# Kernel optimization log

Hardware: AMD Instinct MI355X
Metric: run time of the kernel (lower is better)

## Reference

```python
import jax, jax.numpy as jnp
import numpy as np


def setup_inputs() -> dict:
    key = jax.random.key(0)
    kx, kq, kk, kv = jax.random.split(key, 4)
    B, S, D_IN, H, D_OUT = 2, 2048, 768, 12, 64
    scale = 0.02
    return {
        "x": jax.random.normal(kx, (B, S, D_IN), dtype=jnp.float32),
        "Wq": jax.random.normal(kq, (H, D_IN, D_OUT), dtype=jnp.float32) * scale,
        "Wk": jax.random.normal(kk, (H, D_IN, D_OUT), dtype=jnp.float32) * scale,
        "Wv": jax.random.normal(kv, (H, D_IN, D_OUT), dtype=jnp.float32) * scale,
    }


def reference(x, Wq, Wk, Wv):
    # x: [B, S, d_in]; Wq/Wk/Wv: [H, d_in, d_out] (stacked per-head Linear weights, no bias)
    B, S, _ = x.shape
    H, _, d_out = Wq.shape
    q = jnp.einsum("bsd,hde->bhse", x, Wq)  # [B, H, S, d_out]
    k = jnp.einsum("bsd,hde->bhse", x, Wk)
    v = jnp.einsum("bsd,hde->bhse", x, Wv)
    scores = jnp.einsum("bhse,bhte->bhst", q, k) / jnp.sqrt(jnp.float32(d_out))
    causal = jnp.tril(jnp.ones((S, S), dtype=bool))  # True = keep
    scores = jnp.where(causal, scores, jnp.float32(-jnp.inf))
    attn = jax.nn.softmax(scores, axis=-1)  # dropout = 0.0 -> identity
    ctx = jnp.einsum("bhst,bhte->bhse", attn, v)  # [B, H, S, d_out]
    # concat heads along last dim: [B, S, H*d_out]
    return ctx.transpose(0, 2, 1, 3).reshape(B, S, H * d_out)
```

## Files before the change

### kernel.cpp

```cpp
#include <hip/hip_runtime.h>
#include <hip/hip_bf16.h>


typedef short bf16x8 __attribute__((ext_vector_type(8)));
typedef short bf16x4 __attribute__((ext_vector_type(4)));
typedef float f32x4  __attribute__((ext_vector_type(4)));

#define MFMA16(a, b, c)  __builtin_amdgcn_mfma_f32_16x16x32_bf16((a), (b), (c), 0, 0, 0)
#define MFMAK16(a, b, c) __builtin_amdgcn_mfma_f32_16x16x16bf16_1k((a), (b), (c), 0, 0, 0)
#define SCHED_FENCE() __builtin_amdgcn_sched_barrier(0)
#define MEMBAR() asm volatile("s_barrier" ::: "memory")

static __device__ __forceinline__ unsigned short f2bf(float f) {
    unsigned int u = __builtin_bit_cast(unsigned int, f);
    u += 0x7fffu + ((u >> 16) & 1u);
    return (unsigned short)(u >> 16);
}

static __device__ __forceinline__ int sw(int row, int cb) {
    return (row << 7) + (cb ^ ((row & 7) << 4));
}

static __device__ __forceinline__ void gld16(const void* g, void* l) {
    __builtin_amdgcn_global_load_lds(
        (__attribute__((address_space(1))) void*)g,
        (__attribute__((address_space(3))) void*)l, 16, 0, 0);
}

__global__ __launch_bounds__(256) void prep(const float* __restrict__ x,
                                            const float* __restrict__ Wq,
                                            const float* __restrict__ Wk,
                                            const float* __restrict__ Wv,
                                            char* __restrict__ xb,
                                            char* __restrict__ wtb) {
    __shared__ float tile[64][65];
    const int bid = blockIdx.x;
    const int t = threadIdx.x;
    if (bid < 768) {
        const int stile = bid & 63, ks = bid >> 6;
        const int row = t >> 2, k16 = (t & 3) * 16;
        const float* src = x + (size_t)(stile * 64 + row) * 768 + ks * 64 + k16;
        char* img = xb + ((size_t)stile * 12 + ks) * 8192;
        const float4 v0 = *(const float4*)(src);
        const float4 v1 = *(const float4*)(src + 4);
        const float4 v2 = *(const float4*)(src + 8);
        const float4 v3 = *(const float4*)(src + 12);
        bf16x8 o0, o1;
        o0[0] = (short)f2bf(v0.x); o0[1] = (short)f2bf(v0.y);
        o0[2] = (short)f2bf(v0.z); o0[3] = (short)f2bf(v0.w);
        o0[4] = (short)f2bf(v1.x); o0[5] = (short)f2bf(v1.y);
        o0[6] = (short)f2bf(v1.z); o0[7] = (short)f2bf(v1.w);
        o1[0] = (short)f2bf(v2.x); o1[1] = (short)f2bf(v2.y);
        o1[2] = (short)f2bf(v2.z); o1[3] = (short)f2bf(v2.w);
        o1[4] = (short)f2bf(v3.x); o1[5] = (short)f2bf(v3.y);
        o1[6] = (short)f2bf(v3.z); o1[7] = (short)f2bf(v3.w);
        *(bf16x8*)(img + sw(row, k16 * 2)) = o0;
        *(bf16x8*)(img + sw(row, k16 * 2 + 16)) = o1;
    } else {
        const int idx = bid - 768;
        const int wh = idx % 36, dt = idx / 36;
        const int w = wh / 12, h = wh % 12;
        const float* W = (w == 0) ? Wq : (w == 1) ? Wk : Wv;
        for (int i = 0; i < 4; ++i) {
            int c = t + i * 256;
            int d = c >> 4, e4 = (c & 15) * 4;
            const float4 v = *(const float4*)(W + (size_t)(h * 768 + dt * 64 + d) * 64 + e4);
            tile[d][e4 + 0] = v.x; tile[d][e4 + 1] = v.y;
            tile[d][e4 + 2] = v.z; tile[d][e4 + 3] = v.w;
        }
        __syncthreads();
        char* img = wtb + ((size_t)(wh * 12) + dt) * 8192;
        for (int i = 0; i < 4; ++i) {
            int c = t + i * 256;
            int e = c >> 4, d4 = (c & 15) * 4;
            ushort4 o;
            o.x = f2bf(tile[d4 + 0][e]); o.y = f2bf(tile[d4 + 1][e]);
            o.z = f2bf(tile[d4 + 2][e]); o.w = f2bf(tile[d4 + 3][e]);
            *(ushort4*)(img + e * 128 + ((d4 * 2) ^ ((e & 7) << 4))) = o;
        }
    }
}

__global__ __launch_bounds__(256) void proj_qkv(const char* __restrict__ xb,
                                                const char* __restrict__ wtb,
                                                unsigned short* __restrict__ q,
                                                unsigned short* __restrict__ ksw,
                                                char* __restrict__ vsw) {
    __shared__ __align__(16) char smem[65536];
    const int stile = blockIdx.x;
    const int h = blockIdx.y;
    const int t = threadIdx.x;
    const int wave = t >> 6, lane = t & 63;
    const int lhi = lane >> 4, llo = lane & 15;
    const int wr = wave >> 1, wc = wave & 1;

    const char* asrc = xb + (size_t)stile * 12 * 8192;

    f32x4 acc[3][2][2] = {};

    #define STAGE(KS, BUF)                                                       \
        do {                                                                     \
            const char* s0 = asrc + (KS) * 8192;                                 \
            char* d0 = smem + (BUF) * 32768;                                     \
            gld16(s0 + t * 16, d0 + t * 16);                                     \
            gld16(s0 + t * 16 + 4096, d0 + t * 16 + 4096);                       \
            for (int w3 = 0; w3 < 3; ++w3) {                                     \
                const char* s1 = wtb + ((size_t)((w3 * 12 + h) * 12) + (KS)) * 8192; \
                char* d1 = smem + (BUF) * 32768 + (1 + w3) * 8192;               \
                gld16(s1 + t * 16, d1 + t * 16);                                 \
                gld16(s1 + t * 16 + 4096, d1 + t * 16 + 4096);                   \
            }                                                                    \
        } while (0)

    STAGE(0, 0);
    __syncthreads();
    int cur = 0;
    for (int ks = 0; ks < 12; ++ks) {
        if (ks < 11) STAGE(ks + 1, cur ^ 1);
        char* Alds = smem + cur * 32768;
        #pragma unroll
        for (int kk = 0; kk < 2; ++kk) {
            bf16x8 a[2];
            #pragma unroll
            for (int m = 0; m < 2; ++m)
                a[m] = *(const bf16x8*)(Alds + sw(wr * 32 + m * 16 + llo, kk * 64 + lhi * 16));
            #pragma unroll
            for (int w3 = 0; w3 < 3; ++w3) {
                char* Blds = Alds + (1 + w3) * 8192;
                #pragma unroll
                for (int n = 0; n < 2; ++n) {
                    bf16x8 b = *(const bf16x8*)(Blds + sw(wc * 32 + n * 16 + llo, kk * 64 + lhi * 16));
                    #pragma unroll
                    for (int m = 0; m < 2; ++m)
                        acc[w3][m][n] = MFMA16(a[m], b, acc[w3][m][n]);
                }
            }
        }
        __syncthreads();
        cur ^= 1;
    }
    #undef STAGE

    const float SCALE_Q = 0.18033688011112042f;
    const int bglob = stile >> 5, ktile = stile & 31;
    const int bh = bglob * 12 + h;
    #pragma unroll
    for (int m = 0; m < 2; ++m)
        for (int n = 0; n < 2; ++n)
            for (int r = 0; r < 4; ++r) {
                int s = (stile * 64 + wr * 32 + m * 16 + lhi * 4 + r) & 2047;
                int e = wc * 32 + n * 16 + llo;
                q[(size_t)(bh * 2048 + s) * 64 + e] = f2bf(acc[0][m][n][r] * SCALE_Q);
            }
    unsigned short* kdst = ksw + ((size_t)bh * 32 + ktile) * 4096;
    #pragma unroll
    for (int m = 0; m < 2; ++m)
        for (int n = 0; n < 2; ++n)
            for (int r = 0; r < 4; ++r) {
                int kk = wr * 32 + m * 16 + lhi * 4 + r;
                int e = wc * 32 + n * 16 + llo;
                kdst[kk * 64 + (e ^ ((kk & 7) << 3))] = f2bf(acc[1][m][n][r]);
            }
    char* vtimg = smem;
    __syncthreads();
    #pragma unroll
    for (int m = 0; m < 2; ++m)
        for (int n = 0; n < 2; ++n)
            for (int r = 0; r < 4; ++r) {
                int kk = wr * 32 + m * 16 + lhi * 4 + r;
                int e = wc * 32 + n * 16 + llo;
                int pos = (((kk >> 2) & 3) * 32 + (kk >> 4) * 8 + (kk & 3) * 2) ^ ((e & 7) << 4);
                *(unsigned short*)(vtimg + e * 128 + pos) = f2bf(acc[2][m][n][r]);
            }
    __syncthreads();
    {
        char* dst = vsw + ((size_t)bh * 32 + ktile) * 8192;
        #pragma unroll
        for (int i = 0; i < 2; ++i)
            *(float4*)(dst + t * 16 + i * 4096) =
                *(const float4*)(vtimg + t * 16 + i * 4096);
    }
}

__global__ __launch_bounds__(256) void attn(const unsigned short* __restrict__ Q,
                                            const char* __restrict__ Ksw,
                                            const char* __restrict__ Vsw,
                                            float* __restrict__ out,
                                            float* __restrict__ Obuf,
                                            float* __restrict__ mlbuf) {
    __shared__ __align__(16) char smem[32768];
    const int t = threadIdx.x, wave = t >> 6, lane = t & 63;
    const int lhi = lane >> 4, llo = lane & 15;
    const int bid = blockIdx.x;
    const int xcd = bid & 7, slot = bid >> 3;
    const int bh = xcd + 8 * (slot % 3);
    const int j = slot / 3;
    int qt, kts, kte, part = 0;
    bool split;
    if (j < 16)       { qt = 16 + j; part = 0; kts = 0;  kte = 15; split = true;  }
    else if (j == 16) { qt = 15;               kts = 0;  kte = 15; split = false; }
    else if (j == 17) { qt = 31;     part = 1; kts = 16; kte = 31; split = true;  }
    else {
        const int g = (j - 18) >> 1;
        const int s = 15 - g;
        if (((j - 18) & 1) == 0) { qt = s - 1;            kts = 0;  kte = qt; split = false; }
        else                     { qt = s + 15; part = 1; kts = 16; kte = qt; split = true;  }
    }
    const unsigned short* Qg = Q + (size_t)bh * 2048 * 64;
    const char* Kg = Ksw + (size_t)bh * 32 * 8192;
    const char* Vg = Vsw + (size_t)bh * 32 * 8192;

    const int q0 = qt * 64 + wave * 16;
    bf16x8 qa[2];
    #pragma unroll
    for (int kk = 0; kk < 2; ++kk)
        qa[kk] = *(const bf16x8*)(Qg + (size_t)(q0 + llo) * 64 + kk * 32 + lhi * 8);

    f32x4 acc[4] = {};
    float m_r = -1e30f, l_r = 0.f;

    #define ASTAGE(KT, BUF)                                              \
        do {                                                             \
            const char* ks_ = Kg + (size_t)(KT) * 8192;                  \
            const char* vs_ = Vg + (size_t)(KT) * 8192;                  \
            char* kd = smem + (BUF) * 8192;                              \
            char* vd = smem + 16384 + (BUF) * 8192;                      \
            gld16(ks_ + t * 16, kd + t * 16);                            \
            gld16(ks_ + t * 16 + 4096, kd + t * 16 + 4096);              \
            gld16(vs_ + t * 16, vd + t * 16);                            \
            gld16(vs_ + t * 16 + 4096, vd + t * 16 + 4096);              \
        } while (0)

    ASTAGE(kts, 0);
    SCHED_FENCE();
    int cur = 0;
    for (int kt = kts; kt <= kte; ++kt) {
        if (kt < kte) ASTAGE(kt + 1, cur ^ 1);
        SCHED_FENCE();
        if (kt < kte) asm volatile("s_waitcnt vmcnt(4)" ::: "memory");
        else          asm volatile("s_waitcnt vmcnt(0)" ::: "memory");
        MEMBAR();
        SCHED_FENCE();
        char* Kb = smem + cur * 8192;
        char* Vb = smem + 16384 + cur * 8192;

        f32x4 sc[4];
        __builtin_amdgcn_s_setprio(1);
        #pragma unroll
        for (int n = 0; n < 4; ++n) {
            f32x4 z = {};
            #pragma unroll
            for (int kk = 0; kk < 2; ++kk) {
                bf16x8 bk = *(const bf16x8*)(Kb + sw(n * 16 + llo, kk * 64 + lhi * 16));
                z = MFMA16(bk, qa[kk], z);
            }
            sc[n] = z;
        }
        __builtin_amdgcn_s_setprio(0);
        bf16x8 vfr[4][2];
        #pragma unroll
        for (int n = 0; n < 4; ++n) {
            const int row = n * 16 + llo;
            vfr[n][0] = *(const bf16x8*)(Vb + sw(row, lhi * 32));
            vfr[n][1] = *(const bf16x8*)(Vb + sw(row, lhi * 32 + 16));
        }
        if (kt == qt) {
            #pragma unroll
            for (int n = 0; n < 4; ++n)
                #pragma unroll
                for (int r = 0; r < 4; ++r)
                    if (kt * 64 + n * 16 + lhi * 4 + r > q0 + llo) sc[n][r] = -1e30f;
        }
        float pmax = fmaxf(
            fmaxf(fmaxf(fmaxf(sc[0][0], sc[0][1]), fmaxf(sc[0][2], sc[0][3])),
                  fmaxf(fmaxf(sc[1][0], sc[1][1]), fmaxf(sc[1][2], sc[1][3]))),
            fmaxf(fmaxf(fmaxf(sc[2][0], sc[2][1]), fmaxf(sc[2][2], sc[2][3])),
                  fmaxf(fmaxf(sc[3][0], sc[3][1]), fmaxf(sc[3][2], sc[3][3]))));
        if (__any(pmax > m_r + 8.0f)) {
            float tm = fmaxf(pmax, __shfl_xor(pmax, 16, 64));
            tm = fmaxf(tm, __shfl_xor(tm, 32, 64));
            float nm = fmaxf(m_r, tm);
            float corr = exp2f(m_r - nm);
            m_r = nm;
            l_r *= corr;
            #pragma unroll
            for (int n = 0; n < 4; ++n)
                #pragma unroll
                for (int r = 0; r < 4; ++r) acc[n][r] *= corr;
        }
        bf16x4 pf[4];
        float ps = 0.f;
        #pragma unroll
        for (int kb = 0; kb < 4; ++kb) {
            float p0 = exp2f(sc[kb][0] - m_r), p1 = exp2f(sc[kb][1] - m_r);
            float p2 = exp2f(sc[kb][2] - m_r), p3 = exp2f(sc[kb][3] - m_r);
            ps += (p0 + p1) + (p2 + p3);
            unsigned int w0, w1;
            asm("v_cvt_pk_bf16_f32 %0, %1, %2" : "=v"(w0) : "v"(p0), "v"(p1));
            asm("v_cvt_pk_bf16_f32 %0, %1, %2" : "=v"(w1) : "v"(p2), "v"(p3));
            unsigned long long u = ((unsigned long long)w1 << 32) | w0;
            pf[kb] = __builtin_bit_cast(bf16x4, u);
        }
        l_r += ps;
        __builtin_amdgcn_s_setprio(1);
        #pragma unroll
        for (int n = 0; n < 4; ++n) {
            f32x4 a = acc[n];
            a = MFMAK16(__builtin_shufflevector(vfr[n][0], vfr[n][0], 0, 1, 2, 3), pf[0], a);
            a = MFMAK16(__builtin_shufflevector(vfr[n][0], vfr[n][0], 4, 5, 6, 7), pf[1], a);
            a = MFMAK16(__builtin_shufflevector(vfr[n][1], vfr[n][1], 0, 1, 2, 3), pf[2], a);
            a = MFMAK16(__builtin_shufflevector(vfr[n][1], vfr[n][1], 4, 5, 6, 7), pf[3], a);
            acc[n] = a;
        }
        __builtin_amdgcn_s_setprio(0);
        SCHED_FENCE();
        if (kt < kte) MEMBAR();
        cur ^= 1;
    }
    #undef ASTAGE
    l_r += __shfl_xor(l_r, 16, 64);
    l_r += __shfl_xor(l_r, 32, 64);
    if (split) {
        const int p = ((bh * 16) + (qt - 16)) * 2 + part;
        float* Ob = Obuf + (size_t)p * 4096;
        const int qrow = wave * 16 + llo;
        #pragma unroll
        for (int n = 0; n < 4; ++n) {
            float4 o;
            o.x = acc[n][0]; o.y = acc[n][1]; o.z = acc[n][2]; o.w = acc[n][3];
            *(float4*)(Ob + qrow * 64 + n * 16 + lhi * 4) = o;
        }
        if (lhi == 0) {
            float2 ml; ml.x = m_r; ml.y = l_r;
            *(float2*)(mlbuf + (size_t)p * 128 + qrow * 2) = ml;
        }
    } else {
        const float inv = 1.0f / l_r;
        const int b = bh / 12, h = bh - b * 12;
        #pragma unroll
        for (int n = 0; n < 4; ++n) {
            float4 o;
            o.x = acc[n][0] * inv; o.y = acc[n][1] * inv;
            o.z = acc[n][2] * inv; o.w = acc[n][3] * inv;
            *(float4*)(out + (size_t)(b * 2048 + q0 + llo) * 768 + h * 64 + n * 16 + lhi * 4) = o;
        }
    }
}

__global__ __launch_bounds__(256) void combine(const float* __restrict__ Obuf,
                                               const float* __restrict__ mlbuf,
                                               float* __restrict__ out) {
    const int bid = blockIdx.x;
    const int bh = bid % 24, qt = 16 + bid / 24;
    const int b = bh / 12, h = bh - b * 12;
    const int t = threadIdx.x;
    const int r = t >> 2, c0 = (t & 3) * 16;
    const int p0 = ((bh * 16) + (qt - 16)) * 2;
    const float2 ml0 = *(const float2*)(mlbuf + (size_t)p0 * 128 + r * 2);
    const float2 ml1 = *(const float2*)(mlbuf + (size_t)(p0 + 1) * 128 + r * 2);
    const float mm = fmaxf(ml0.x, ml1.x);
    const float w0 = exp2f(ml0.x - mm), w1 = exp2f(ml1.x - mm);
    const float inv = 1.0f / (ml0.y * w0 + ml1.y * w1);
    const float* s0 = Obuf + (size_t)p0 * 4096 + r * 64 + c0;
    const float* s1 = s0 + 4096;
    float* dst = out + (size_t)(b * 2048 + qt * 64 + r) * 768 + h * 64 + c0;
    #pragma unroll
    for (int i = 0; i < 4; ++i) {
        const float4 a = *(const float4*)(s0 + i * 4);
        const float4 c = *(const float4*)(s1 + i * 4);
        float4 o;
        o.x = (a.x * w0 + c.x * w1) * inv;
        o.y = (a.y * w0 + c.y * w1) * inv;
        o.z = (a.z * w0 + c.z * w1) * inv;
        o.w = (a.w * w0 + c.w * w1) * inv;
        *(float4*)(dst + i * 4) = o;
    }
}

extern "C" void kernel_launch(void* const* d_in, const int* in_sizes, int n_in,
                              void* d_out, int out_size, void* d_ws, size_t ws_size,
                              hipStream_t stream) {
    const float* x  = (const float*)d_in[0];
    const float* Wq = (const float*)d_in[1];
    const float* Wk = (const float*)d_in[2];
    const float* Wv = (const float*)d_in[3];
    float* out = (float*)d_out;

    char* ws = (char*)d_ws;
    char*           wtb   = ws;
    unsigned short* q     = (unsigned short*)(ws + 3538944);
    unsigned short* ksw   = (unsigned short*)(ws + 9830400);
    char*           vsw   = (char*)(ws + 16121856);
    char*           xb    = (char*)(ws + 22413312);
    float*          Obuf  = (float*)(ws + 28704768);
    float*          mlbuf = (float*)(ws + 41287680);

    hipLaunchKernelGGL(prep, dim3(1200), dim3(256), 0, stream, x, Wq, Wk, Wv, xb, wtb);
    hipLaunchKernelGGL(proj_qkv, dim3(64, 12), dim3(256), 0, stream,
                       xb, wtb, q, ksw, vsw);
    hipLaunchKernelGGL(attn, dim3(1152), dim3(256), 0, stream,
                       q, (const char*)ksw, vsw, out, Obuf, mlbuf);
    hipLaunchKernelGGL(combine, dim3(384), dim3(256), 0, stream, Obuf, mlbuf, out);
}
```

Baseline: 69.73 us.

## Pre-pack projection operands in MFMA fragment order and load directly from global

The conversion kernel now writes x and the transposed weights in per-lane MFMA fragment order, so each lane's bf16x8 operand sits contiguously at lane*16 within a 1 KB fragment block. The projection GEMM then drops its double-buffered LDS staging and barriers and loads A/B fragments straight from global memory into registers with a fully unrolled K loop. This removes the LDS traffic and per-step synchronization, at the cost of more register pressure and exposed global-load latency with no explicit prefetch. Reuse across waves now comes through L1/L2 instead of shared memory.

```diff
diff --git a/kernel.cpp b/kernel.cpp
--- a/kernel.cpp
+++ b/kernel.cpp
@@ -54,8 +54,14 @@
         o1[2] = (short)f2bf(v2.z); o1[3] = (short)f2bf(v2.w);
         o1[4] = (short)f2bf(v3.x); o1[5] = (short)f2bf(v3.y);
         o1[6] = (short)f2bf(v3.z); o1[7] = (short)f2bf(v3.w);
-        *(bf16x8*)(img + sw(row, k16 * 2)) = o0;
-        *(bf16x8*)(img + sw(row, k16 * 2 + 16)) = o1;
+        const int wr = row >> 5, m = (row >> 4) & 1, llo = row & 15;
+        const int f0 = wr * 4 + m * 2 + (k16 >> 5);
+        const int ln0 = ((k16 >> 3) & 3) * 16 + llo;
+        const int k8 = k16 + 8;
+        const int f1 = wr * 4 + m * 2 + (k8 >> 5);
+        const int ln1 = ((k8 >> 3) & 3) * 16 + llo;
+        *(bf16x8*)(img + f0 * 1024 + ln0 * 16) = o0;
+        *(bf16x8*)(img + f1 * 1024 + ln1 * 16) = o1;
     } else {
         const int idx = bid - 768;
         const int wh = idx % 36, dt = idx / 36;
@@ -70,23 +76,28 @@
         }
         __syncthreads();
         char* img = wtb + ((size_t)(wh * 12) + dt) * 8192;
-        for (int i = 0; i < 4; ++i) {
+        #pragma unroll
+        for (int i = 0; i < 2; ++i) {
             int c = t + i * 256;
-            int e = c >> 4, d4 = (c & 15) * 4;
-            ushort4 o;
-            o.x = f2bf(tile[d4 + 0][e]); o.y = f2bf(tile[d4 + 1][e]);
-            o.z = f2bf(tile[d4 + 2][e]); o.w = f2bf(tile[d4 + 3][e]);
-            *(ushort4*)(img + e * 128 + ((d4 * 2) ^ ((e & 7) << 4))) = o;
-        }
-    }
-}
-
-__global__ __launch_bounds__(256) void proj_qkv(const char* __restrict__ xb,
-                                                const char* __restrict__ wtb,
+            int fB = c >> 6, lane = c & 63;
+            int wc = fB >> 2, n = (fB >> 1) & 1, kk = fB & 1;
+            int lhi = lane >> 4, llo = lane & 15;
+            int e = wc * 32 + n * 16 + llo;
+            int d0 = kk * 32 + lhi * 8;
+            bf16x8 o;
+            #pragma unroll
+            for (int jj = 0; jj < 8; ++jj) o[jj] = (short)f2bf(tile[d0 + jj][e]);
+            *(bf16x8*)(img + fB * 1024 + lane * 16) = o;
+        }
+    }
+}
+
+__global__ __launch_bounds__(256) void proj_qkv(const char* __restrict__ xbF,
+                                                const char* __restrict__ wtbF,
                                                 unsigned short* __restrict__ q,
                                                 unsigned short* __restrict__ ksw,
                                                 char* __restrict__ vsw) {
-    __shared__ __align__(16) char smem[65536];
+    __shared__ __align__(16) char vtimg[8192];
     const int stile = blockIdx.x;
     const int h = blockIdx.y;
     const int t = threadIdx.x;
@@ -94,52 +105,44 @@
     const int lhi = lane >> 4, llo = lane & 15;
     const int wr = wave >> 1, wc = wave & 1;
 
-    const char* asrc = xb + (size_t)stile * 12 * 8192;
+    const char* abase = xbF + (size_t)stile * 12 * 8192 + (wr * 4) * 1024 + lane * 16;
+    const char* bbase0 = wtbF + ((size_t)((0 * 12 + h) * 12)) * 8192 + (wc * 4) * 1024 + lane * 16;
+    const char* bbase1 = wtbF + ((size_t)((1 * 12 + h) * 12)) * 8192 + (wc * 4) * 1024 + lane * 16;
+    const char* bbase2 = wtbF + ((size_t)((2 * 12 + h) * 12)) * 8192 + (wc * 4) * 1024 + lane * 16;
 
     f32x4 acc[3][2][2] = {};
 
-    #define STAGE(KS, BUF)                                                       \
-        do {                                                                     \
-            const char* s0 = asrc + (KS) * 8192;                                 \
-            char* d0 = smem + (BUF) * 32768;                                     \
-            gld16(s0 + t * 16, d0 + t * 16);                                     \
-            gld16(s0 + t * 16 + 4096, d0 + t * 16 + 4096);                       \
-            for (int w3 = 0; w3 < 3; ++w3) {                                     \
-                const char* s1 = wtb + ((size_t)((w3 * 12 + h) * 12) + (KS)) * 8192; \
-                char* d1 = smem + (BUF) * 32768 + (1 + w3) * 8192;               \
-                gld16(s1 + t * 16, d1 + t * 16);                                 \
-                gld16(s1 + t * 16 + 4096, d1 + t * 16 + 4096);                   \
-            }                                                                    \
-        } while (0)
-
-    STAGE(0, 0);
-    __syncthreads();
-    int cur = 0;
+    #pragma unroll
     for (int ks = 0; ks < 12; ++ks) {
-        if (ks < 11) STAGE(ks + 1, cur ^ 1);
-        char* Alds = smem + cur * 32768;
-        #pragma unroll
-        for (int kk = 0; kk < 2; ++kk) {
-            bf16x8 a[2];
-            #pragma unroll
-            for (int m = 0; m < 2; ++m)
-                a[m] = *(const bf16x8*)(Alds + sw(wr * 32 + m * 16 + llo, kk * 64 + lhi * 16));
-            #pragma unroll
-            for (int w3 = 0; w3 < 3; ++w3) {
-                char* Blds = Alds + (1 + w3) * 8192;
+        bf16x8 a[2][2], b0[2][2], b1[2][2], b2[2][2];
+        const char* ap = abase + ks * 8192;
+        #pragma unroll
+        for (int m = 0; m < 2; ++m)
+            #pragma unroll
+            for (int kk = 0; kk < 2; ++kk)
+                a[m][kk] = *(const bf16x8*)(ap + (m * 2 + kk) * 1024);
+        const char* bp0 = bbase0 + ks * 8192;
+        const char* bp1 = bbase1 + ks * 8192;
+        const char* bp2 = bbase2 + ks * 8192;
+        #pragma unroll
+        for (int n = 0; n < 2; ++n)
+            #pragma unroll
+            for (int kk = 0; kk < 2; ++kk) {
+                b0[n][kk] = *(const bf16x8*)(bp0 + (n * 2 + kk) * 1024);
+                b1[n][kk] = *(const bf16x8*)(bp1 + (n * 2 + kk) * 1024);
+                b2[n][kk] = *(const bf16x8*)(bp2 + (n * 2 + kk) * 1024);
+            }
+        #pragma unroll
+        for (int kk = 0; kk < 2; ++kk)
+            #pragma unroll
+            for (int n = 0; n < 2; ++n)
                 #pragma unroll
-                for (int n = 0; n < 2; ++n) {
-                    bf16x8 b = *(const bf16x8*)(Blds + sw(wc * 32 + n * 16 + llo, kk * 64 + lhi * 16));
-                    #pragma unroll
-                    for (int m = 0; m < 2; ++m)
-                        acc[w3][m][n] = MFMA16(a[m], b, acc[w3][m][n]);
+                for (int m = 0; m < 2; ++m) {
+                    acc[0][m][n] = MFMA16(a[m][kk], b0[n][kk], acc[0][m][n]);
+                    acc[1][m][n] = MFMA16(a[m][kk], b1[n][kk], acc[1][m][n]);
+                    acc[2][m][n] = MFMA16(a[m][kk], b2[n][kk], acc[2][m][n]);
                 }
-            }
-        }
-        __syncthreads();
-        cur ^= 1;
-    }
-    #undef STAGE
+    }
 
     const float SCALE_Q = 0.18033688011112042f;
     const int bglob = stile >> 5, ktile = stile & 31;
@@ -161,8 +164,6 @@
                 int e = wc * 32 + n * 16 + llo;
                 kdst[kk * 64 + (e ^ ((kk & 7) << 3))] = f2bf(acc[1][m][n][r]);
             }
-    char* vtimg = smem;
-    __syncthreads();
     #pragma unroll
     for (int m = 0; m < 2; ++m)
         for (int n = 0; n < 2; ++n)
```

Measured after the change: 72.90 us. 4.6% more time.
